# Performance work log

Measured on AMD Instinct MI355X. Metric: run time of the kernel, lower is better.

Reference implementation:

```python
import jax, jax.numpy as jnp
import numpy as np

N_NODES = 100000
N_EDGES = 1600000
DIM = 128
N_LAYERS = 3
BN_EPS = 1e-5


def setup_inputs() -> dict:
    key = jax.random.key(0)
    ks = jax.random.split(key, 8)
    x = jax.random.normal(ks[0], (N_NODES, DIM), dtype=jnp.float32)
    edge_index = jax.random.randint(ks[1], (2, N_EDGES), 0, N_NODES, dtype=jnp.int64)
    # Stacked per-layer params (all layers are DIM->DIM since input_dim==hidden_dim)
    W1 = jax.random.normal(ks[2], (N_LAYERS, DIM, DIM), dtype=jnp.float32) * 0.05
    b1 = jnp.zeros((N_LAYERS, DIM), dtype=jnp.float32)
    gamma = jnp.ones((N_LAYERS, DIM), dtype=jnp.float32)
    beta = jnp.zeros((N_LAYERS, DIM), dtype=jnp.float32)
    rmean = jnp.zeros((N_LAYERS, DIM), dtype=jnp.float32)
    rvar = jnp.ones((N_LAYERS, DIM), dtype=jnp.float32)
    W2 = jax.random.normal(ks[3], (N_LAYERS, DIM, DIM), dtype=jnp.float32) * 0.05
    b2 = jnp.zeros((N_LAYERS, DIM), dtype=jnp.float32)
    return {"x": x, "edge_index": edge_index, "W1": W1, "b1": b1,
            "gamma": gamma, "beta": beta, "rmean": rmean, "rvar": rvar,
            "W2": W2, "b2": b2}


def _gin_layer(h, src, dst, W1_l, b1_l, g_l, be_l, m_l, v_l, W2_l, b2_l):
    # adj_t @ h : sum of neighbor (src) features into dst nodes
    agg = jax.ops.segment_sum(h[src], dst, num_segments=N_NODES)
    h = h + agg  # (1 + eps) * x + agg, eps = 0
    h = h @ W1_l + b1_l
    # BatchNorm1d (inference mode, running stats)
    h = (h - m_l) * jax.lax.rsqrt(v_l + BN_EPS) * g_l + be_l
    h = jax.nn.relu(h)
    h = h @ W2_l + b2_l
    return jax.nn.relu(h)


def reference(x, edge_index, W1, b1, gamma, beta, rmean, rvar, W2, b2):
    src, dst = edge_index[0], edge_index[1]
    h = x
    for l in range(N_LAYERS):
        h = _gin_layer(h, src, dst, W1[l], b1[l], gamma[l], beta[l],
                       rmean[l], rvar[l], W2[l], b2[l])
        # dropout is identity in eval mode
    return jax.nn.log_softmax(h, axis=-1)
```

## Files before the change

### kernel.cpp

```cpp
#include <hip/hip_runtime.h>
#include <hip/hip_bf16.h>
#include <cstdint>

#define DIM 128
#define ASTR 136
#define WSTR 136
#define NBKT 512
#define BCAP 4608
#define ECHUNK 2500

typedef __bf16 bf16x8 __attribute__((ext_vector_type(8)));
typedef float  f32x4  __attribute__((ext_vector_type(4)));
typedef unsigned short u16x8 __attribute__((ext_vector_type(8)));
typedef unsigned short u16x4 __attribute__((ext_vector_type(4)));

__device__ __forceinline__ unsigned short f2bf(float f) {
    union { float f; unsigned u; } x; x.f = f;
    unsigned r = x.u + 0x7fffu + ((x.u >> 16) & 1u);
    return (unsigned short)(r >> 16);
}
__device__ __forceinline__ float2 bfpair2f(unsigned v) {
    union { unsigned u; float f; } a, b;
    a.u = v << 16;
    b.u = v & 0xffff0000u;
    return make_float2(a.f, b.f);
}

__device__ __forceinline__ void load_edge(const unsigned* __restrict__ eidx,
                                          int e, int E, int is64,
                                          int& s, int& d) {
    if (is64) {
        s = (int)eidx[2 * (size_t)e];
        d = (int)eidx[2 * ((size_t)E + (size_t)e)];
    } else {
        s = (int)eidx[(size_t)e];
        d = (int)eidx[(size_t)E + (size_t)e];
    }
}

__global__ __launch_bounds__(256) void prep_bin(
    const float* __restrict__ x,
    const float* __restrict__ W1, const float* __restrict__ W2,
    const float* __restrict__ b1, const float* __restrict__ g,
    const float* __restrict__ be, const float* __restrict__ m,
    const float* __restrict__ v, const unsigned* __restrict__ eidx,
    unsigned short* __restrict__ Wt, float* __restrict__ affA,
    float* __restrict__ affB, u16x4* __restrict__ P,
    int* __restrict__ gpos, unsigned* __restrict__ binned,
    int M, int E, int bblk, int xblk, int wblk)
{
    __shared__ int cnt[NBKT];
    __shared__ int bas[NBKT];
    __shared__ unsigned pk[ECHUNK];
    __shared__ unsigned short bkL[ECHUNK];
    const int b = blockIdx.x, t = threadIdx.x;

    if (b < bblk) {
        int is64 = 1;
        #pragma unroll 4
        for (int i = 0; i < 32; ++i)
            if (eidx[2 * i + 1] != 0u) { is64 = 0; break; }
        const int e0 = b * ECHUNK;
        int n = E - e0; if (n > ECHUNK) n = ECHUNK;

        for (int i = t; i < NBKT; i += 256) cnt[i] = 0;
        __syncthreads();
        for (int i = t; i < n; i += 256) {
            int s, d; load_edge(eidx, e0 + i, E, is64, s, d);
            int bk = d >> 8;
            pk[i] = ((unsigned)s << 8) | (unsigned)(d & 255);
            bkL[i] = (unsigned short)bk;
            atomicAdd(&cnt[bk], 1);
        }
        __syncthreads();
        for (int i = t; i < NBKT; i += 256) {
            int c = cnt[i];
            bas[i] = c ? atomicAdd(&gpos[i], c) : 0;
        }
        __syncthreads();
        for (int i = t; i < n; i += 256) {
            int bk = bkL[i];
            int slot = atomicAdd(&bas[bk], 1);
            if (slot < BCAP)
                binned[(size_t)bk * BCAP + slot] = pk[i];
        }
    } else if (b < bblk + xblk) {
        int id = (b - bblk) * 256 + t;
        if (id < M * 32) {
            float4 vv = ((const float4*)x)[id];
            u16x4 o;
            o[0] = f2bf(vv.x); o[1] = f2bf(vv.y);
            o[2] = f2bf(vv.z); o[3] = f2bf(vv.w);
            P[id] = o;
        }
    } else if (b < bblk + xblk + wblk) {
        int id = (b - bblk - xblk) * 256 + t;
        int l = id / 32768;
        int r = id - l * 32768;
        int w = r >> 14;
        int idx = r & 16383;
        int k = idx >> 7, n = idx & 127;
        const float* src = (w ? W2 : W1) + (size_t)l * 16384;
        Wt[(size_t)id - idx + ((size_t)n * 128 + k)] = f2bf(src[k * 128 + n]);
    } else {
        for (int id = t; id < 3 * DIM; id += 256) {
            float A = g[id] * rsqrtf(v[id] + 1e-5f);
            affA[id] = A;
            affB[id] = (b1[id] - m[id]) * A + be[id];
        }
    }
}

__global__ __launch_bounds__(256) void bucket_fill(
    const unsigned* __restrict__ binned, const int* __restrict__ gpos,
    int* __restrict__ off, int* __restrict__ csr, int M)
{
    __shared__ unsigned bl[BCAP];
    __shared__ int sc[NBKT];
    __shared__ int cntL[256];
    __shared__ int sh[256];
    __shared__ int posL[256];
    const int b = blockIdx.x;
    const int t = threadIdx.x;

    sc[t]       = min(gpos[t], BCAP);
    sc[t + 256] = min(gpos[t + 256], BCAP);
    const int nb = min(gpos[b], BCAP);
    __syncthreads();
    for (int ofs = 1; ofs < NBKT; ofs <<= 1) {
        int a0 = (t >= ofs) ? sc[t - ofs] : 0;
        int a1 = sc[t + 256 - ofs];
        __syncthreads();
        sc[t] += a0; sc[t + 256] += a1;
        __syncthreads();
    }
    const int base = sc[b] - nb;

    for (int i = t; i < nb; i += 256)
        bl[i] = binned[(size_t)b * BCAP + i];
    cntL[t] = 0;
    __syncthreads();
    for (int i = t; i < nb; i += 256)
        atomicAdd(&cntL[bl[i] & 255], 1);
    __syncthreads();
    sh[t] = cntL[t];
    __syncthreads();
    #pragma unroll
    for (int ofs = 1; ofs < 256; ofs <<= 1) {
        int add = (t >= ofs) ? sh[t - ofs] : 0;
        __syncthreads();
        sh[t] += add;
        __syncthreads();
    }
    int excl = sh[t] - cntL[t];
    int node = b * 256 + t;
    if (node <= M) off[node] = base + excl;
    posL[t] = excl;
    __syncthreads();
    for (int i = t; i < nb; i += 256) {
        unsigned vv = bl[i];
        int slot = atomicAdd(&posL[vv & 255], 1);
        csr[base + slot] = (int)(vv >> 8);
    }
}

__device__ __forceinline__ void addpair(float2& a, unsigned v) {
    float2 p = bfpair2f(v);
    a.x += p.x; a.y += p.y;
}

__global__ __launch_bounds__(256) void gather_v(
    const uint4* __restrict__ Hv,
    const int* __restrict__ off, const int* __restrict__ csr,
    uint4* __restrict__ AGv, int M)
{
    int node = (blockIdx.x * 256 + threadIdx.x) >> 6;
    if (node >= M) return;
    int lane = threadIdx.x & 63;
    int q = lane >> 4, li = lane & 15;

    float2 acc[4];
    acc[0] = acc[1] = acc[2] = acc[3] = make_float2(0.f, 0.f);
    if (q == 0) {
        uint4 w = Hv[(size_t)node * 16 + li];
        acc[0] = bfpair2f(w.x); acc[1] = bfpair2f(w.y);
        acc[2] = bfpair2f(w.z); acc[3] = bfpair2f(w.w);
    }

    const int beg = off[node], end = off[node + 1];
    for (int jb = beg; jb < end; jb += 32) {
        int idx[8];
        uint4 w[8];
        #pragma unroll
        for (int u = 0; u < 8; ++u) {
            idx[u] = jb + u * 4 + q;
            int ic = idx[u] < end ? idx[u] : end - 1;
            int s = csr[ic];
            w[u] = Hv[(size_t)s * 16 + li];
        }
        #pragma unroll
        for (int u = 0; u < 8; ++u) {
            if (idx[u] >= end) { w[u].x = 0; w[u].y = 0; w[u].z = 0; w[u].w = 0; }
            addpair(acc[0], w[u].x);
            addpair(acc[1], w[u].y);
            addpair(acc[2], w[u].z);
            addpair(acc[3], w[u].w);
        }
    }

    #pragma unroll
    for (int k = 0; k < 4; ++k) {
        acc[k].x += __shfl_xor(acc[k].x, 16);
        acc[k].y += __shfl_xor(acc[k].y, 16);
        acc[k].x += __shfl_xor(acc[k].x, 32);
        acc[k].y += __shfl_xor(acc[k].y, 32);
    }
    if (q == 0) {
        uint4 o;
        o.x = (unsigned)f2bf(acc[0].x) | ((unsigned)f2bf(acc[0].y) << 16);
        o.y = (unsigned)f2bf(acc[1].x) | ((unsigned)f2bf(acc[1].y) << 16);
        o.z = (unsigned)f2bf(acc[2].x) | ((unsigned)f2bf(acc[2].y) << 16);
        o.w = (unsigned)f2bf(acc[3].x) | ((unsigned)f2bf(acc[3].y) << 16);
        AGv[(size_t)node * 16 + li] = o;
    }
}

template<int LAST>
__global__ __launch_bounds__(256) void fused_layer(
    const unsigned short* __restrict__ AGGb,
    const unsigned short* __restrict__ W1t,
    const unsigned short* __restrict__ W2t,
    const float* __restrict__ affA, const float* __restrict__ affB,
    const float* __restrict__ b2, void* __restrict__ OUTp, int M)
{
    __shared__ unsigned short H1s[64 * ASTR];
    __shared__ unsigned short Wsub[128 * WSTR];
    const int t = threadIdx.x;
    const int row0 = blockIdx.x * 64;
    const int w = t >> 6;
    const int lane = t & 63;
    const int lm = lane & 15;
    const int quad = lane >> 4;

    const unsigned short* ap = AGGb + (size_t)(row0 + w * 16 + lm) * DIM;
    bf16x8 afr[4];
    #pragma unroll
    for (int kc = 0; kc < 4; ++kc)
        afr[kc] = *(const bf16x8*)(ap + kc * 32 + quad * 8);

    #pragma unroll
    for (int i = 0; i < 16; ++i) {
        int idx = t + 256 * i;
        int n = idx >> 5, kc = idx & 31;
        *(ushort4*)&Wsub[n * WSTR + kc * 4] = ((const ushort4*)W1t)[idx];
    }
    __syncthreads();

    f32x4 acc[8];
    #pragma unroll
    for (int i = 0; i < 8; ++i) { f32x4 z = {0.f, 0.f, 0.f, 0.f}; acc[i] = z; }
    #pragma unroll
    for (int kc = 0; kc < 4; ++kc) {
        int k0 = kc * 32 + quad * 8;
        bf16x8 a = afr[kc];
        #pragma unroll
        for (int tt = 0; tt < 8; ++tt) {
            bf16x8 b = *(const bf16x8*)&Wsub[(tt * 16 + lm) * WSTR + k0];
            acc[tt] = __builtin_amdgcn_mfma_f32_16x16x32_bf16(a, b, acc[tt], 0, 0, 0);
        }
    }

    #pragma unroll
    for (int tt = 0; tt < 8; ++tt) {
        int c = tt * 16 + lm;
        float aA = affA[c], aB = affB[c];
        #pragma unroll
        for (int r = 0; r < 4; ++r) {
            float h = fmaxf(acc[tt][r] * aA + aB, 0.f);
            H1s[(w * 16 + quad * 4 + r) * ASTR + c] = f2bf(h);
        }
    }
    __syncthreads();
    #pragma unroll
    for (int i = 0; i < 16; ++i) {
        int idx = t + 256 * i;
        int n = idx >> 5, kc = idx & 31;
        *(ushort4*)&Wsub[n * WSTR + kc * 4] = ((const ushort4*)W2t)[idx];
    }
    __syncthreads();

    const int arow = w * 16 + lm;
    f32x4 acc2[8];
    #pragma unroll
    for (int i = 0; i < 8; ++i) { f32x4 z = {0.f, 0.f, 0.f, 0.f}; acc2[i] = z; }
    #pragma unroll
    for (int kc = 0; kc < 4; ++kc) {
        int k0 = kc * 32 + quad * 8;
        bf16x8 a = *(const bf16x8*)&H1s[arow * ASTR + k0];
        #pragma unroll
        for (int tt = 0; tt < 8; ++tt) {
            bf16x8 b = *(const bf16x8*)&Wsub[(tt * 16 + lm) * WSTR + k0];
            acc2[tt] = __builtin_amdgcn_mfma_f32_16x16x32_bf16(a, b, acc2[tt], 0, 0, 0);
        }
    }

    float v[8][4];
    #pragma unroll
    for (int tt = 0; tt < 8; ++tt) {
        int c = tt * 16 + lm;
        float bb = b2[c];
        #pragma unroll
        for (int r = 0; r < 4; ++r)
            v[tt][r] = fmaxf(acc2[tt][r] + bb, 0.f);
    }

    if (!LAST) {
        unsigned short* OUT = (unsigned short*)OUTp;
        #pragma unroll
        for (int tt = 0; tt < 8; ++tt) {
            int c = tt * 16 + lm;
            #pragma unroll
            for (int r = 0; r < 4; ++r) {
                int gr = row0 + w * 16 + quad * 4 + r;
                if (gr < M) OUT[(size_t)gr * DIM + c] = f2bf(v[tt][r]);
            }
        }
    } else {
        float* OUT = (float*)OUTp;
        #pragma unroll
        for (int r = 0; r < 4; ++r) {
            float mm = v[0][r];
            #pragma unroll
            for (int tt = 1; tt < 8; ++tt) mm = fmaxf(mm, v[tt][r]);
            #pragma unroll
            for (int ofs = 1; ofs < 16; ofs <<= 1)
                mm = fmaxf(mm, __shfl_xor(mm, ofs));
            float ss = 0.f;
            #pragma unroll
            for (int tt = 0; tt < 8; ++tt) ss += __expf(v[tt][r] - mm);
            #pragma unroll
            for (int ofs = 1; ofs < 16; ofs <<= 1)
                ss += __shfl_xor(ss, ofs);
            float lse = mm + __logf(ss);
            int gr = row0 + w * 16 + quad * 4 + r;
            if (gr < M) {
                #pragma unroll
                for (int tt = 0; tt < 8; ++tt)
                    OUT[(size_t)gr * DIM + tt * 16 + lm] = v[tt][r] - lse;
            }
        }
    }
}

static inline size_t align256(size_t v) { return (v + 255) & ~(size_t)255; }

extern "C" void kernel_launch(void* const* d_in, const int* in_sizes, int n_in,
                              void* d_out, int out_size, void* d_ws, size_t ws_size,
                              hipStream_t stream) {
    const float*    x     = (const float*)d_in[0];
    const unsigned* eidx  = (const unsigned*)d_in[1];
    const float*    W1    = (const float*)d_in[2];
    const float*    b1    = (const float*)d_in[3];
    const float*    gamma = (const float*)d_in[4];
    const float*    beta  = (const float*)d_in[5];
    const float*    rmean = (const float*)d_in[6];
    const float*    rvar  = (const float*)d_in[7];
    const float*    W2    = (const float*)d_in[8];
    const float*    b2    = (const float*)d_in[9];

    const int M = in_sizes[0] / DIM;
    const int E = in_sizes[1] / 2;
    const size_t hbf_bytes = (size_t)M * DIM * 2;

    float* out = (float*)d_out;
    char*  ws  = (char*)d_ws;

    size_t o = 0;
    unsigned short* Wt = (unsigned short*)(ws + o); o = align256(o + (size_t)3 * 2 * 16384 * 2);
    float* affA = (float*)(ws + o);                 o = align256(o + 3 * DIM * 4);
    float* affB = (float*)(ws + o);                 o = align256(o + 3 * DIM * 4);
    int* gpos  = (int*)(ws + o);                    o = align256(o + NBKT * 4);
    int* off   = (int*)(ws + o);                    o = align256(o + ((size_t)M + 1) * 4);
    int* csr   = (int*)(ws + o);                    o = align256(o + (size_t)E * 4);
    unsigned short* Q = (unsigned short*)(ws + o);  o = align256(o + hbf_bytes);
    unsigned short* P = (unsigned short*)(ws + o);  o = align256(o + hbf_bytes);
    unsigned* binned = (unsigned*)Q;

    const int bblk = (E + ECHUNK - 1) / ECHUNK;
    const int xblk = (M * 32 + 255) / 256;
    const int wblk = (3 * 2 * 16384 + 255) / 256;

    hipMemsetAsync(gpos, 0, NBKT * 4, stream);
    prep_bin<<<bblk + xblk + wblk + 1, 256, 0, stream>>>(
        x, W1, W2, b1, gamma, beta, rmean, rvar, eidx,
        Wt, affA, affB, (u16x4*)P, gpos, binned, M, E, bblk, xblk, wblk);
    bucket_fill<<<NBKT, 256, 0, stream>>>(binned, gpos, off, csr, M);

    const int gat_blocks  = (M + 3) / 4;
    const int fuse_blocks = (M + 63) / 64;

    gather_v<<<gat_blocks, 256, 0, stream>>>((const uint4*)P, off, csr,
                                             (uint4*)Q, M);
    fused_layer<0><<<fuse_blocks, 256, 0, stream>>>(
        Q, Wt + 0 * 16384, Wt + 1 * 16384,
        affA + 0 * DIM, affB + 0 * DIM, b2 + 0 * DIM, (void*)P, M);
    gather_v<<<gat_blocks, 256, 0, stream>>>((const uint4*)P, off, csr,
                                             (uint4*)Q, M);
    fused_layer<0><<<fuse_blocks, 256, 0, stream>>>(
        Q, Wt + 2 * 16384, Wt + 3 * 16384,
        affA + 1 * DIM, affB + 1 * DIM, b2 + 1 * DIM, (void*)P, M);
    gather_v<<<gat_blocks, 256, 0, stream>>>((const uint4*)P, off, csr,
                                             (uint4*)Q, M);
    fused_layer<1><<<fuse_blocks, 256, 0, stream>>>(
        Q, Wt + 4 * 16384, Wt + 5 * 16384,
        affA + 2 * DIM, affB + 2 * DIM, b2 + 2 * DIM, (void*)out, M);
}
```

Baseline: 406.0 us.

## Fuse neighbor gather into the per-layer MLP kernel via shared memory

```diff
diff --git a/kernel.cpp b/kernel.cpp
--- a/kernel.cpp
+++ b/kernel.cpp
@@ -169,71 +169,16 @@
     a.x += p.x; a.y += p.y;
 }
 
-__global__ __launch_bounds__(256) void gather_v(
+template<int LAST>
+__global__ __launch_bounds__(256, 3) void gin_layer(
     const uint4* __restrict__ Hv,
     const int* __restrict__ off, const int* __restrict__ csr,
-    uint4* __restrict__ AGv, int M)
-{
-    int node = (blockIdx.x * 256 + threadIdx.x) >> 6;
-    if (node >= M) return;
-    int lane = threadIdx.x & 63;
-    int q = lane >> 4, li = lane & 15;
-
-    float2 acc[4];
-    acc[0] = acc[1] = acc[2] = acc[3] = make_float2(0.f, 0.f);
-    if (q == 0) {
-        uint4 w = Hv[(size_t)node * 16 + li];
-        acc[0] = bfpair2f(w.x); acc[1] = bfpair2f(w.y);
-        acc[2] = bfpair2f(w.z); acc[3] = bfpair2f(w.w);
-    }
-
-    const int beg = off[node], end = off[node + 1];
-    for (int jb = beg; jb < end; jb += 32) {
-        int idx[8];
-        uint4 w[8];
-        #pragma unroll
-        for (int u = 0; u < 8; ++u) {
-            idx[u] = jb + u * 4 + q;
-            int ic = idx[u] < end ? idx[u] : end - 1;
-            int s = csr[ic];
-            w[u] = Hv[(size_t)s * 16 + li];
-        }
-        #pragma unroll
-        for (int u = 0; u < 8; ++u) {
-            if (idx[u] >= end) { w[u].x = 0; w[u].y = 0; w[u].z = 0; w[u].w = 0; }
-            addpair(acc[0], w[u].x);
-            addpair(acc[1], w[u].y);
-            addpair(acc[2], w[u].z);
-            addpair(acc[3], w[u].w);
-        }
-    }
-
-    #pragma unroll
-    for (int k = 0; k < 4; ++k) {
-        acc[k].x += __shfl_xor(acc[k].x, 16);
-        acc[k].y += __shfl_xor(acc[k].y, 16);
-        acc[k].x += __shfl_xor(acc[k].x, 32);
-        acc[k].y += __shfl_xor(acc[k].y, 32);
-    }
-    if (q == 0) {
-        uint4 o;
-        o.x = (unsigned)f2bf(acc[0].x) | ((unsigned)f2bf(acc[0].y) << 16);
-        o.y = (unsigned)f2bf(acc[1].x) | ((unsigned)f2bf(acc[1].y) << 16);
-        o.z = (unsigned)f2bf(acc[2].x) | ((unsigned)f2bf(acc[2].y) << 16);
-        o.w = (unsigned)f2bf(acc[3].x) | ((unsigned)f2bf(acc[3].y) << 16);
-        AGv[(size_t)node * 16 + li] = o;
-    }
-}
-
-template<int LAST>
-__global__ __launch_bounds__(256) void fused_layer(
-    const unsigned short* __restrict__ AGGb,
     const unsigned short* __restrict__ W1t,
     const unsigned short* __restrict__ W2t,
     const float* __restrict__ affA, const float* __restrict__ affB,
     const float* __restrict__ b2, void* __restrict__ OUTp, int M)
 {
-    __shared__ unsigned short H1s[64 * ASTR];
+    __shared__ unsigned short Hblk[64 * ASTR];
     __shared__ unsigned short Wsub[128 * WSTR];
     const int t = threadIdx.x;
     const int row0 = blockIdx.x * 64;
@@ -242,18 +187,68 @@
     const int lm = lane & 15;
     const int quad = lane >> 4;
 
-    const unsigned short* ap = AGGb + (size_t)(row0 + w * 16 + lm) * DIM;
-    bf16x8 afr[4];
-    #pragma unroll
-    for (int kc = 0; kc < 4; ++kc)
-        afr[kc] = *(const bf16x8*)(ap + kc * 32 + quad * 8);
-
     #pragma unroll
     for (int i = 0; i < 16; ++i) {
         int idx = t + 256 * i;
         int n = idx >> 5, kc = idx & 31;
         *(ushort4*)&Wsub[n * WSTR + kc * 4] = ((const ushort4*)W1t)[idx];
     }
+
+    #pragma unroll 1
+    for (int i = 0; i < 16; ++i) {
+        const int node = row0 + w * 16 + i;
+        float2 acc[4];
+        acc[0] = acc[1] = acc[2] = acc[3] = make_float2(0.f, 0.f);
+        if (node < M) {
+            if (quad == 0) {
+                uint4 s0 = Hv[(size_t)node * 16 + lm];
+                acc[0] = bfpair2f(s0.x); acc[1] = bfpair2f(s0.y);
+                acc[2] = bfpair2f(s0.z); acc[3] = bfpair2f(s0.w);
+            }
+            const int beg = off[node], end = off[node + 1];
+            for (int jb = beg; jb < end; jb += 32) {
+                int idxv[8];
+                uint4 wv[8];
+                #pragma unroll
+                for (int u = 0; u < 8; ++u) {
+                    idxv[u] = jb + u * 4 + quad;
+                    int ic = idxv[u] < end ? idxv[u] : end - 1;
+                    int s = csr[ic];
+                    wv[u] = Hv[(size_t)s * 16 + lm];
+                }
+                #pragma unroll
+                for (int u = 0; u < 8; ++u) {
+                    if (idxv[u] >= end) { wv[u].x = 0; wv[u].y = 0; wv[u].z = 0; wv[u].w = 0; }
+                    addpair(acc[0], wv[u].x);
+                    addpair(acc[1], wv[u].y);
+                    addpair(acc[2], wv[u].z);
+                    addpair(acc[3], wv[u].w);
+                }
+            }
+            #pragma unroll
+            for (int k = 0; k < 4; ++k) {
+                acc[k].x += __shfl_xor(acc[k].x, 16);
+                acc[k].y += __shfl_xor(acc[k].y, 16);
+                acc[k].x += __shfl_xor(acc[k].x, 32);
+                acc[k].y += __shfl_xor(acc[k].y, 32);
+            }
+        }
+        if (quad == 0) {
+            uint4 o;
+            o.x = (unsigned)f2bf(acc[0].x) | ((unsigned)f2bf(acc[0].y) << 16);
+            o.y = (unsigned)f2bf(acc[1].x) | ((unsigned)f2bf(acc[1].y) << 16);
+            o.z = (unsigned)f2bf(acc[2].x) | ((unsigned)f2bf(acc[2].y) << 16);
+            o.w = (unsigned)f2bf(acc[3].x) | ((unsigned)f2bf(acc[3].y) << 16);
+            *(uint4*)&Hblk[(size_t)(w * 16 + i) * ASTR + lm * 8] = o;
+        }
+    }
+
+    bf16x8 afr[4];
+    const unsigned short* arowp = &Hblk[(w * 16 + lm) * ASTR];
+    #pragma unroll
+    for (int kc = 0; kc < 4; ++kc)
+        afr[kc] = *(const bf16x8*)(arowp + kc * 32 + quad * 8);
+
     __syncthreads();
 
     f32x4 acc[8];
@@ -277,7 +272,7 @@
         #pragma unroll
         for (int r = 0; r < 4; ++r) {
             float h = fmaxf(acc[tt][r] * aA + aB, 0.f);
-            H1s[(w * 16 + quad * 4 + r) * ASTR + c] = f2bf(h);
+            Hblk[(w * 16 + quad * 4 + r) * ASTR + c] = f2bf(h);
         }
     }
     __syncthreads();
@@ -296,7 +291,7 @@
     #pragma unroll
     for (int kc = 0; kc < 4; ++kc) {
         int k0 = kc * 32 + quad * 8;
-        bf16x8 a = *(const bf16x8*)&H1s[arow * ASTR + k0];
+        bf16x8 a = *(const bf16x8*)&Hblk[arow * ASTR + k0];
         #pragma unroll
         for (int tt = 0; tt < 8; ++tt) {
             bf16x8 b = *(const bf16x8*)&Wsub[(tt * 16 + lm) * WSTR + k0];
@@ -396,22 +391,15 @@
         Wt, affA, affB, (u16x4*)P, gpos, binned, M, E, bblk, xblk, wblk);
     bucket_fill<<<NBKT, 256, 0, stream>>>(binned, gpos, off, csr, M);
 
-    const int gat_blocks  = (M + 3) / 4;
     const int fuse_blocks = (M + 63) / 64;
 
-    gather_v<<<gat_blocks, 256, 0, stream>>>((const uint4*)P, off, csr,
-                                             (uint4*)Q, M);
-    fused_layer<0><<<fuse_blocks, 256, 0, stream>>>(
-        Q, Wt + 0 * 16384, Wt + 1 * 16384,
-        affA + 0 * DIM, affB + 0 * DIM, b2 + 0 * DIM, (void*)P, M);
-    gather_v<<<gat_blocks, 256, 0, stream>>>((const uint4*)P, off, csr,
-                                             (uint4*)Q, M);
-    fused_layer<0><<<fuse_blocks, 256, 0, stream>>>(
-        Q, Wt + 2 * 16384, Wt + 3 * 16384,
+    gin_layer<0><<<fuse_blocks, 256, 0, stream>>>(
+        (const uint4*)P, off, csr, Wt + 0 * 16384, Wt + 1 * 16384,
+        affA + 0 * DIM, affB + 0 * DIM, b2 + 0 * DIM, (void*)Q, M);
+    gin_layer<0><<<fuse_blocks, 256, 0, stream>>>(
+        (const uint4*)Q, off, csr, Wt + 2 * 16384, Wt + 3 * 16384,
         affA + 1 * DIM, affB + 1 * DIM, b2 + 1 * DIM, (void*)P, M);
-    gather_v<<<gat_blocks, 256, 0, stream>>>((const uint4*)P, off, csr,
-                                             (uint4*)Q, M);
-    fused_layer<1><<<fuse_blocks, 256, 0, stream>>>(
-        Q, Wt + 4 * 16384, Wt + 5 * 16384,
+    gin_layer<1><<<fuse_blocks, 256, 0, stream>>>(
+        (const uint4*)P, off, csr, Wt + 4 * 16384, Wt + 5 * 16384,
         affA + 2 * DIM, affB + 2 * DIM, b2 + 2 * DIM, (void*)out, M);
 }
```

Result: slower. 487.6 us (+20.1%).

## Replace bucketed CSR build with global histogram, scan, and atomic scatter

Applied to the files above, without the earlier changes.

```diff
diff --git a/kernel.cpp b/kernel.cpp
--- a/kernel.cpp
+++ b/kernel.cpp
@@ -5,9 +5,6 @@
 #define DIM 128
 #define ASTR 136
 #define WSTR 136
-#define NBKT 512
-#define BCAP 4608
-#define ECHUNK 2500
 
 typedef __bf16 bf16x8 __attribute__((ext_vector_type(8)));
 typedef float  f32x4  __attribute__((ext_vector_type(4)));
@@ -26,19 +23,15 @@
     return make_float2(a.f, b.f);
 }
 
-__device__ __forceinline__ void load_edge(const unsigned* __restrict__ eidx,
-                                          int e, int E, int is64,
-                                          int& s, int& d) {
-    if (is64) {
-        s = (int)eidx[2 * (size_t)e];
-        d = (int)eidx[2 * ((size_t)E + (size_t)e)];
-    } else {
-        s = (int)eidx[(size_t)e];
-        d = (int)eidx[(size_t)E + (size_t)e];
-    }
-}
-
-__global__ __launch_bounds__(256) void prep_bin(
+__device__ __forceinline__ int detect_is64(const unsigned* __restrict__ eidx) {
+    int is64 = 1;
+    #pragma unroll 4
+    for (int i = 0; i < 32; ++i)
+        if (eidx[2 * i + 1] != 0u) { is64 = 0; break; }
+    return is64;
+}
+
+__global__ __launch_bounds__(256) void prep(
     const float* __restrict__ x,
     const float* __restrict__ W1, const float* __restrict__ W2,
     const float* __restrict__ b1, const float* __restrict__ g,
@@ -46,46 +39,30 @@
     const float* __restrict__ v, const unsigned* __restrict__ eidx,
     unsigned short* __restrict__ Wt, float* __restrict__ affA,
     float* __restrict__ affB, u16x4* __restrict__ P,
-    int* __restrict__ gpos, unsigned* __restrict__ binned,
-    int M, int E, int bblk, int xblk, int wblk)
-{
-    __shared__ int cnt[NBKT];
-    __shared__ int bas[NBKT];
-    __shared__ unsigned pk[ECHUNK];
-    __shared__ unsigned short bkL[ECHUNK];
+    int* __restrict__ cnt,
+    int M, int E, int hblk, int xblk, int wblk)
+{
     const int b = blockIdx.x, t = threadIdx.x;
 
-    if (b < bblk) {
-        int is64 = 1;
-        #pragma unroll 4
-        for (int i = 0; i < 32; ++i)
-            if (eidx[2 * i + 1] != 0u) { is64 = 0; break; }
-        const int e0 = b * ECHUNK;
-        int n = E - e0; if (n > ECHUNK) n = ECHUNK;
-
-        for (int i = t; i < NBKT; i += 256) cnt[i] = 0;
-        __syncthreads();
-        for (int i = t; i < n; i += 256) {
-            int s, d; load_edge(eidx, e0 + i, E, is64, s, d);
-            int bk = d >> 8;
-            pk[i] = ((unsigned)s << 8) | (unsigned)(d & 255);
-            bkL[i] = (unsigned short)bk;
-            atomicAdd(&cnt[bk], 1);
-        }
-        __syncthreads();
-        for (int i = t; i < NBKT; i += 256) {
-            int c = cnt[i];
-            bas[i] = c ? atomicAdd(&gpos[i], c) : 0;
-        }
-        __syncthreads();
-        for (int i = t; i < n; i += 256) {
-            int bk = bkL[i];
-            int slot = atomicAdd(&bas[bk], 1);
-            if (slot < BCAP)
-                binned[(size_t)bk * BCAP + slot] = pk[i];
-        }
-    } else if (b < bblk + xblk) {
-        int id = (b - bblk) * 256 + t;
+    if (b < hblk) {
+        const int is64 = detect_is64(eidx);
+        const int per = (E + hblk - 1) / hblk;
+        const int e0 = b * per;
+        int n = E - e0; if (n > per) n = per; if (n < 0) n = 0;
+        if (is64) {
+            const uint2* dstp = (const uint2*)eidx;
+            for (int i = t; i < n; i += 256) {
+                int d = (int)dstp[(size_t)E + e0 + i].x;
+                atomicAdd(&cnt[d], 1);
+            }
+        } else {
+            for (int i = t; i < n; i += 256) {
+                int d = (int)eidx[(size_t)E + e0 + i];
+                atomicAdd(&cnt[d], 1);
+            }
+        }
+    } else if (b < hblk + xblk) {
+        int id = (b - hblk) * 256 + t;
         if (id < M * 32) {
             float4 vv = ((const float4*)x)[id];
             u16x4 o;
@@ -93,8 +70,8 @@
             o[2] = f2bf(vv.z); o[3] = f2bf(vv.w);
             P[id] = o;
         }
-    } else if (b < bblk + xblk + wblk) {
-        int id = (b - bblk - xblk) * 256 + t;
+    } else if (b < hblk + xblk + wblk) {
+        int id = (b - hblk - xblk) * 256 + t;
         int l = id / 32768;
         int r = id - l * 32768;
         int w = r >> 14;
@@ -111,56 +88,89 @@
     }
 }
 
-__global__ __launch_bounds__(256) void bucket_fill(
-    const unsigned* __restrict__ binned, const int* __restrict__ gpos,
-    int* __restrict__ off, int* __restrict__ csr, int M)
-{
-    __shared__ unsigned bl[BCAP];
-    __shared__ int sc[NBKT];
-    __shared__ int cntL[256];
+__global__ __launch_bounds__(256) void scan1(
+    const int* __restrict__ cnt, int* __restrict__ off,
+    int* __restrict__ aux, int M)
+{
     __shared__ int sh[256];
-    __shared__ int posL[256];
-    const int b = blockIdx.x;
+    const int b = blockIdx.x, t = threadIdx.x;
+    const int base = b * 1024 + t * 4;
+    int v[4], s = 0;
+    #pragma unroll
+    for (int j = 0; j < 4; ++j) {
+        int i = base + j;
+        v[j] = (i < M) ? cnt[i] : 0;
+        s += v[j];
+    }
+    sh[t] = s;
+    __syncthreads();
+    #pragma unroll
+    for (int ofs = 1; ofs < 256; ofs <<= 1) {
+        int a = (t >= ofs) ? sh[t - ofs] : 0;
+        __syncthreads();
+        sh[t] += a;
+        __syncthreads();
+    }
+    int run = sh[t] - s;
+    #pragma unroll
+    for (int j = 0; j < 4; ++j) {
+        int i = base + j;
+        if (i < M) off[i] = run;
+        run += v[j];
+    }
+    if (t == 255) aux[b] = sh[255];
+}
+
+__global__ __launch_bounds__(256) void scan_fix(
+    int* __restrict__ off, const int* __restrict__ aux,
+    int nb, int M, int E)
+{
+    __shared__ int sh[256];
+    __shared__ int ex[128];
     const int t = threadIdx.x;
-
-    sc[t]       = min(gpos[t], BCAP);
-    sc[t + 256] = min(gpos[t + 256], BCAP);
-    const int nb = min(gpos[b], BCAP);
-    __syncthreads();
-    for (int ofs = 1; ofs < NBKT; ofs <<= 1) {
-        int a0 = (t >= ofs) ? sc[t - ofs] : 0;
-        int a1 = sc[t + 256 - ofs];
+    int v = (t < nb) ? aux[t] : 0;
+    sh[t] = v;
+    __syncthreads();
+    #pragma unroll
+    for (int ofs = 1; ofs < 256; ofs <<= 1) {
+        int a = (t >= ofs) ? sh[t - ofs] : 0;
         __syncthreads();
-        sc[t] += a0; sc[t + 256] += a1;
+        sh[t] += a;
         __syncthreads();
     }
-    const int base = sc[b] - nb;
-
-    for (int i = t; i < nb; i += 256)
-        bl[i] = binned[(size_t)b * BCAP + i];
-    cntL[t] = 0;
-    __syncthreads();
-    for (int i = t; i < nb; i += 256)
-        atomicAdd(&cntL[bl[i] & 255], 1);
-    __syncthreads();
-    sh[t] = cntL[t];
-    __syncthreads();
-    #pragma unroll
-    for (int ofs = 1; ofs < 256; ofs <<= 1) {
-        int add = (t >= ofs) ? sh[t - ofs] : 0;
-        __syncthreads();
-        sh[t] += add;
-        __syncthreads();
-    }
-    int excl = sh[t] - cntL[t];
-    int node = b * 256 + t;
-    if (node <= M) off[node] = base + excl;
-    posL[t] = excl;
-    __syncthreads();
-    for (int i = t; i < nb; i += 256) {
-        unsigned vv = bl[i];
-        int slot = atomicAdd(&posL[vv & 255], 1);
-        csr[base + slot] = (int)(vv >> 8);
+    if (t < nb) ex[t] = sh[t] - v;
+    __syncthreads();
+    const int i = blockIdx.x * 256 + t;
+    if (i < M) off[i] += ex[i >> 10];
+    if (i == 0) off[M] = E;
+}
+
+__global__ __launch_bounds__(256) void scatter(
+    const unsigned* __restrict__ eidx, const int* __restrict__ off,
+    int* __restrict__ cnt, int* __restrict__ csr, int E, int sblk)
+{
+    const int b = blockIdx.x, t = threadIdx.x;
+    const int is64 = detect_is64(eidx);
+    const int per = (E + sblk - 1) / sblk;
+    const int e0 = b * per;
+    int n = E - e0; if (n > per) n = per; if (n < 0) n = 0;
+    if (is64) {
+        const uint2* p = (const uint2*)eidx;
+        for (int i = t; i < n; i += 256) {
+            int e = e0 + i;
+            int s = (int)p[(size_t)e].x;
+            int d = (int)p[(size_t)E + e].x;
+            int slot = atomicSub(&cnt[d], 1) - 1;
+            csr[off[d] + slot] = s;
+        }
+    } else {
+        for (int i = t; i < n; i += 256) {
+            int e = e0 + i;
+            int s = (int)eidx[(size_t)e];
+            int d = (int)eidx[(size_t)E + e];
+            int slot = atomicSub(&cnt[d], 1) - 1;
+            csr[off[d] + slot] = s;
+        }
     }
 }
 
@@ -379,22 +389,27 @@
     unsigned short* Wt = (unsigned short*)(ws + o); o = align256(o + (size_t)3 * 2 * 16384 * 2);
     float* affA = (float*)(ws + o);                 o = align256(o + 3 * DIM * 4);
     float* affB = (float*)(ws + o);                 o = align256(o + 3 * DIM * 4);
-    int* gpos  = (int*)(ws + o);                    o = align256(o + NBKT * 4);
+    int* cnt   = (int*)(ws + o);                    o = align256(o + (size_t)M * 4);
+    int* aux   = (int*)(ws + o);                    o = align256(o + 128 * 4);
     int* off   = (int*)(ws + o);                    o = align256(o + ((size_t)M + 1) * 4);
     int* csr   = (int*)(ws + o);                    o = align256(o + (size_t)E * 4);
     unsigned short* Q = (unsigned short*)(ws + o);  o = align256(o + hbf_bytes);
     unsigned short* P = (unsigned short*)(ws + o);  o = align256(o + hbf_bytes);
-    unsigned* binned = (unsigned*)Q;
-
-    const int bblk = (E + ECHUNK - 1) / ECHUNK;
+
+    const int hblk = 2048;
     const int xblk = (M * 32 + 255) / 256;
     const int wblk = (3 * 2 * 16384 + 255) / 256;
-
-    hipMemsetAsync(gpos, 0, NBKT * 4, stream);
-    prep_bin<<<bblk + xblk + wblk + 1, 256, 0, stream>>>(
+    const int nb1  = (M + 1023) / 1024;
+    const int fixb = (M + 255) / 256;
+    const int sblk = 2048;
+
+    hipMemsetAsync(cnt, 0, (size_t)M * 4, stream);
+    prep<<<hblk + xblk + wblk + 1, 256, 0, stream>>>(
         x, W1, W2, b1, gamma, beta, rmean, rvar, eidx,
-        Wt, affA, affB, (u16x4*)P, gpos, binned, M, E, bblk, xblk, wblk);
-    bucket_fill<<<NBKT, 256, 0, stream>>>(binned, gpos, off, csr, M);
+        Wt, affA, affB, (u16x4*)P, cnt, M, E, hblk, xblk, wblk);
+    scan1<<<nb1, 256, 0, stream>>>(cnt, off, aux, M);
+    scan_fix<<<fixb, 256, 0, stream>>>(off, aux, nb1, M, E);
+    scatter<<<sblk, 256, 0, stream>>>(eidx, off, cnt, csr, E, sblk);
 
     const int gat_blocks  = (M + 3) / 4;
     const int fuse_blocks = (M + 63) / 64;
```

After: 533.6 us. 31.4% more time.

## Read weights directly from global in non-final layers and rebin edges in two passes

Applied to the files above, without the earlier changes.

```diff
diff --git a/kernel.cpp b/kernel.cpp
--- a/kernel.cpp
+++ b/kernel.cpp
@@ -7,7 +7,7 @@
 #define WSTR 136
 #define NBKT 512
 #define BCAP 4608
-#define ECHUNK 2500
+#define ECHUNK 10000
 
 typedef __bf16 bf16x8 __attribute__((ext_vector_type(8)));
 typedef float  f32x4  __attribute__((ext_vector_type(4)));
@@ -24,6 +24,14 @@
     a.u = v << 16;
     b.u = v & 0xffff0000u;
     return make_float2(a.f, b.f);
+}
+
+__device__ __forceinline__ int detect_is64(const unsigned* __restrict__ eidx) {
+    int is64 = 1;
+    #pragma unroll 4
+    for (int i = 0; i < 32; ++i)
+        if (eidx[2 * i + 1] != 0u) { is64 = 0; break; }
+    return is64;
 }
 
 __device__ __forceinline__ void load_edge(const unsigned* __restrict__ eidx,
@@ -51,38 +59,39 @@
 {
     __shared__ int cnt[NBKT];
     __shared__ int bas[NBKT];
-    __shared__ unsigned pk[ECHUNK];
-    __shared__ unsigned short bkL[ECHUNK];
     const int b = blockIdx.x, t = threadIdx.x;
 
     if (b < bblk) {
-        int is64 = 1;
-        #pragma unroll 4
-        for (int i = 0; i < 32; ++i)
-            if (eidx[2 * i + 1] != 0u) { is64 = 0; break; }
+        const int is64 = detect_is64(eidx);
         const int e0 = b * ECHUNK;
         int n = E - e0; if (n > ECHUNK) n = ECHUNK;
 
         for (int i = t; i < NBKT; i += 256) cnt[i] = 0;
+        __syncthreads();
+        if (is64) {
+            for (int i = t; i < n; i += 256) {
+                int d = (int)eidx[2 * ((size_t)E + e0 + i)];
+                atomicAdd(&cnt[d >> 8], 1);
+            }
+        } else {
+            for (int i = t; i < n; i += 256) {
+                int d = (int)eidx[(size_t)E + e0 + i];
+                atomicAdd(&cnt[d >> 8], 1);
+            }
+        }
+        __syncthreads();
+        for (int i = t; i < NBKT; i += 256) {
+            int c = cnt[i];
+            bas[i] = c ? atomicAdd(&gpos[i], c) : 0;
+        }
         __syncthreads();
         for (int i = t; i < n; i += 256) {
             int s, d; load_edge(eidx, e0 + i, E, is64, s, d);
             int bk = d >> 8;
-            pk[i] = ((unsigned)s << 8) | (unsigned)(d & 255);
-            bkL[i] = (unsigned short)bk;
-            atomicAdd(&cnt[bk], 1);
-        }
-        __syncthreads();
-        for (int i = t; i < NBKT; i += 256) {
-            int c = cnt[i];
-            bas[i] = c ? atomicAdd(&gpos[i], c) : 0;
-        }
-        __syncthreads();
-        for (int i = t; i < n; i += 256) {
-            int bk = bkL[i];
             int slot = atomicAdd(&bas[bk], 1);
             if (slot < BCAP)
-                binned[(size_t)bk * BCAP + slot] = pk[i];
+                binned[(size_t)bk * BCAP + slot] =
+                    ((unsigned)s << 8) | (unsigned)(d & 255);
         }
     } else if (b < bblk + xblk) {
         int id = (b - bblk) * 256 + t;
@@ -225,13 +234,86 @@
     }
 }
 
-template<int LAST>
-__global__ __launch_bounds__(256) void fused_layer(
+__global__ __launch_bounds__(256, 8) void fused_bf(
     const unsigned short* __restrict__ AGGb,
     const unsigned short* __restrict__ W1t,
     const unsigned short* __restrict__ W2t,
     const float* __restrict__ affA, const float* __restrict__ affB,
-    const float* __restrict__ b2, void* __restrict__ OUTp, int M)
+    const float* __restrict__ b2, unsigned short* __restrict__ OUT, int M)
+{
+    __shared__ unsigned short H1s[64 * ASTR];
+    const int t = threadIdx.x;
+    const int row0 = blockIdx.x * 64;
+    const int w = t >> 6;
+    const int lane = t & 63;
+    const int lm = lane & 15;
+    const int quad = lane >> 4;
+
+    const unsigned short* ap = AGGb + (size_t)(row0 + w * 16 + lm) * DIM;
+    bf16x8 afr[4];
+    #pragma unroll
+    for (int kc = 0; kc < 4; ++kc)
+        afr[kc] = *(const bf16x8*)(ap + kc * 32 + quad * 8);
+
+    f32x4 acc[8];
+    #pragma unroll
+    for (int i = 0; i < 8; ++i) { f32x4 z = {0.f, 0.f, 0.f, 0.f}; acc[i] = z; }
+    #pragma unroll
+    for (int kc = 0; kc < 4; ++kc) {
+        int k0 = kc * 32 + quad * 8;
+        bf16x8 a = afr[kc];
+        #pragma unroll
+        for (int tt = 0; tt < 8; ++tt) {
+            bf16x8 b = *(const bf16x8*)&W1t[(size_t)(tt * 16 + lm) * DIM + k0];
+            acc[tt] = __builtin_amdgcn_mfma_f32_16x16x32_bf16(a, b, acc[tt], 0, 0, 0);
+        }
+    }
+
+    #pragma unroll
+    for (int tt = 0; tt < 8; ++tt) {
+        int c = tt * 16 + lm;
+        float aA = affA[c], aB = affB[c];
+        #pragma unroll
+        for (int r = 0; r < 4; ++r) {
+            float h = fmaxf(acc[tt][r] * aA + aB, 0.f);
+            H1s[(w * 16 + quad * 4 + r) * ASTR + c] = f2bf(h);
+        }
+    }
+
+    const int arow = w * 16 + lm;
+    f32x4 acc2[8];
+    #pragma unroll
+    for (int i = 0; i < 8; ++i) { f32x4 z = {0.f, 0.f, 0.f, 0.f}; acc2[i] = z; }
+    #pragma unroll
+    for (int kc = 0; kc < 4; ++kc) {
+        int k0 = kc * 32 + quad * 8;
+        bf16x8 a = *(const bf16x8*)&H1s[arow * ASTR + k0];
+        #pragma unroll
+        for (int tt = 0; tt < 8; ++tt) {
+            bf16x8 b = *(const bf16x8*)&W2t[(size_t)(tt * 16 + lm) * DIM + k0];
+            acc2[tt] = __builtin_amdgcn_mfma_f32_16x16x32_bf16(a, b, acc2[tt], 0, 0, 0);
+        }
+    }
+
+    #pragma unroll
+    for (int tt = 0; tt < 8; ++tt) {
+        int c = tt * 16 + lm;
+        float bb = b2[c];
+        #pragma unroll
+        for (int r = 0; r < 4; ++r) {
+            int gr = row0 + w * 16 + quad * 4 + r;
+            if (gr < M)
+                OUT[(size_t)gr * DIM + c] = f2bf(fmaxf(acc2[tt][r] + bb, 0.f));
+        }
+    }
+}
+
+__global__ __launch_bounds__(256) void fused_last(
+    const unsigned short* __restrict__ AGGb,
+    const unsigned short* __restrict__ W1t,
+    const unsigned short* __restrict__ W2t,
+    const float* __restrict__ affA, const float* __restrict__ affB,
+    const float* __restrict__ b2, float* __restrict__ OUT, int M)
 {
     __shared__ unsigned short H1s[64 * ASTR];
     __shared__ unsigned short Wsub[128 * WSTR];
@@ -314,40 +396,26 @@
             v[tt][r] = fmaxf(acc2[tt][r] + bb, 0.f);
     }
 
-    if (!LAST) {
-        unsigned short* OUT = (unsigned short*)OUTp;
-        #pragma unroll
-        for (int tt = 0; tt < 8; ++tt) {
-            int c = tt * 16 + lm;
+    #pragma unroll
+    for (int r = 0; r < 4; ++r) {
+        float mm = v[0][r];
+        #pragma unroll
+        for (int tt = 1; tt < 8; ++tt) mm = fmaxf(mm, v[tt][r]);
+        #pragma unroll
+        for (int ofs = 1; ofs < 16; ofs <<= 1)
+            mm = fmaxf(mm, __shfl_xor(mm, ofs));
+        float ss = 0.f;
+        #pragma unroll
+        for (int tt = 0; tt < 8; ++tt) ss += __expf(v[tt][r] - mm);
+        #pragma unroll
+        for (int ofs = 1; ofs < 16; ofs <<= 1)
+            ss += __shfl_xor(ss, ofs);
+        float lse = mm + __logf(ss);
+        int gr = row0 + w * 16 + quad * 4 + r;
+        if (gr < M) {
             #pragma unroll
-            for (int r = 0; r < 4; ++r) {
-                int gr = row0 + w * 16 + quad * 4 + r;
-                if (gr < M) OUT[(size_t)gr * DIM + c] = f2bf(v[tt][r]);
-            }
-        }
-    } else {
-        float* OUT = (float*)OUTp;
-        #pragma unroll
-        for (int r = 0; r < 4; ++r) {
-            float mm = v[0][r];
-            #pragma unroll
-            for (int tt = 1; tt < 8; ++tt) mm = fmaxf(mm, v[tt][r]);
-            #pragma unroll
-            for (int ofs = 1; ofs < 16; ofs <<= 1)
-                mm = fmaxf(mm, __shfl_xor(mm, ofs));
-            float ss = 0.f;
-            #pragma unroll
-            for (int tt = 0; tt < 8; ++tt) ss += __expf(v[tt][r] - mm);
-            #pragma unroll
-            for (int ofs = 1; ofs < 16; ofs <<= 1)
-                ss += __shfl_xor(ss, ofs);
-            float lse = mm + __logf(ss);
-            int gr = row0 + w * 16 + quad * 4 + r;
-            if (gr < M) {
-                #pragma unroll
-                for (int tt = 0; tt < 8; ++tt)
-                    OUT[(size_t)gr * DIM + tt * 16 + lm] = v[tt][r] - lse;
-            }
+            for (int tt = 0; tt < 8; ++tt)
+                OUT[(size_t)gr * DIM + tt * 16 + lm] = v[tt][r] - lse;
         }
     }
 }
@@ -401,17 +469,17 @@
 
     gather_v<<<gat_blocks, 256, 0, stream>>>((const uint4*)P, off, csr,
                                              (uint4*)Q, M);
-    fused_layer<0><<<fuse_blocks, 256, 0, stream>>>(
+    fused_bf<<<fuse_blocks, 256, 0, stream>>>(
         Q, Wt + 0 * 16384, Wt + 1 * 16384,
-        affA + 0 * DIM, affB + 0 * DIM, b2 + 0 * DIM, (void*)P, M);
+        affA + 0 * DIM, affB + 0 * DIM, b2 + 0 * DIM, P, M);
     gather_v<<<gat_blocks, 256, 0, stream>>>((const uint4*)P, off, csr,
                                              (uint4*)Q, M);
-    fused_layer<0><<<fuse_blocks, 256, 0, stream>>>(
+    fused_bf<<<fuse_blocks, 256, 0, stream>>>(
         Q, Wt + 2 * 16384, Wt + 3 * 16384,
-        affA + 1 * DIM, affB + 1 * DIM, b2 + 1 * DIM, (void*)P, M);
+        affA + 1 * DIM, affB + 1 * DIM, b2 + 1 * DIM, P, M);
     gather_v<<<gat_blocks, 256, 0, stream>>>((const uint4*)P, off, csr,
                                              (uint4*)Q, M);
-    fused_layer<1><<<fuse_blocks, 256, 0, stream>>>(
+    fused_last<<<fuse_blocks, 256, 0, stream>>>(
         Q, Wt + 4 * 16384, Wt + 5 * 16384,
-        affA + 2 * DIM, affB + 2 * DIM, b2 + 2 * DIM, (void*)out, M);
-}
+        affA + 2 * DIM, affB + 2 * DIM, b2 + 2 * DIM, out, M);
+}
```

New measurement: 513.7 us. 1.27x slower.
